# Performance work log

Measured on AMD Instinct MI355X. Metric: run time of the kernel, lower is better.

The kernel has to match this reference:

```python
import jax, jax.numpy as jnp
import numpy as np

N_NODES = 100000

def setup_inputs() -> dict:
    key = jax.random.key(0)
    k1, k2, k3, k4 = jax.random.split(key, 4)
    B, S, D, H = 50000, 10, 128, 128
    nodes = jax.random.randint(k1, (B,), 0, N_NODES, dtype=jnp.int64 if jax.config.jax_enable_x64 else jnp.int32)
    neigh_idx = jax.random.randint(k2, (B, S), 0, N_NODES, dtype=nodes.dtype)
    feature = jax.random.normal(k3, (N_NODES, D), dtype=jnp.float32)
    weight = jax.random.normal(k4, (2 * D, H), dtype=jnp.float32) * (1.0 / np.sqrt(2 * D))
    return {"nodes": nodes, "neigh_idx": neigh_idx, "feature": feature, "weight": weight}

def reference(nodes, neigh_idx, feature, weight):
    # Mean aggregation over sampled neighbors: [B, S, D] -> [B, D]
    neigh_feats = jnp.mean(feature[neigh_idx], axis=1)
    # Self features: [B, D]
    self_feats = feature[nodes]
    # Concat + linear + ReLU (gcn=False branch)
    combined = jnp.concatenate([self_feats, neigh_feats], axis=1)  # [B, 2D]
    return jax.nn.relu(combined @ weight)  # [B, H]
```

## Files before the change

kernel.cpp:

```cpp
#include <hip/hip_runtime.h>


typedef __attribute__((ext_vector_type(8))) short bf16x8;
typedef __attribute__((ext_vector_type(4))) float f32x4;

__device__ __forceinline__ unsigned short f2bf(float x) {
  unsigned int u = __float_as_uint(x);
  u += 0x7fffu + ((u >> 16) & 1u);
  return (unsigned short)(u >> 16);
}

__global__ void sage_prep_wt2(const float* __restrict__ W,
                              unsigned short* __restrict__ Wt) {
  __shared__ float tile[32][132];
  const int t = threadIdx.x;
  const int kbase = blockIdx.x * 32;
  const float4* w4 = (const float4*)(W + (size_t)kbase * 128);
#pragma unroll
  for (int j = 0; j < 4; ++j) {
    int f4i = t + j * 256;
    float4 v = w4[f4i];
    int flat = f4i << 2;
    int kk = flat >> 7;
    int h  = flat & 127;
    tile[kk][h] = v.x; tile[kk][h + 1] = v.y;
    tile[kk][h + 2] = v.z; tile[kk][h + 3] = v.w;
  }
  __syncthreads();
  const int h  = t >> 1;
  const int kc = (t & 1) * 16;
  unsigned short* dst = &Wt[(size_t)h * 256 + kbase + kc];
#pragma unroll
  for (int j = 0; j < 4; ++j) {
    ushort4 o;
    o.x = f2bf(tile[kc + 4 * j + 0][h]);
    o.y = f2bf(tile[kc + 4 * j + 1][h]);
    o.z = f2bf(tile[kc + 4 * j + 2][h]);
    o.w = f2bf(tile[kc + 4 * j + 3][h]);
    *(ushort4*)&dst[4 * j] = o;
  }
}

__global__ __launch_bounds__(512, 4)
void sage_fused6(const int* __restrict__ nodes,
                 const int* __restrict__ neigh,
                 const float* __restrict__ feat,
                 const unsigned short* __restrict__ Wt,
                 float* __restrict__ out, int B)
{
  constexpr int K = 256, H = 128, S = 10;
  constexpr int TILE = 64;
  constexpr int STR = K + 8;
  __shared__ unsigned short Clds[TILE * STR];

  const int t = threadIdx.x;
  const int block0 = blockIdx.x * TILE;

  {
    const int r   = t >> 5;
    const int sub = t & 31;
    const float4* f4 = (const float4*)feat;

#pragma unroll
    for (int half = 0; half < 4; ++half) {
      const int row = r + half * 16;
      const int b = block0 + row;
      unsigned short* crow = &Clds[row * STR];
      if (b < B) {
        const long srow = (long)nodes[b] * 32;
        float4 sv = f4[srow + sub];

        float ax = 0.f, ay = 0.f, az = 0.f, aw = 0.f;
#pragma unroll
        for (int s = 0; s < S; ++s) {
          const long nrow = (long)neigh[b * S + s] * 32;
          float4 v = f4[nrow + sub];
          ax += v.x; ay += v.y; az += v.z; aw += v.w;
        }
        ushort4 o;
        o.x = f2bf(sv.x); o.y = f2bf(sv.y); o.z = f2bf(sv.z); o.w = f2bf(sv.w);
        *(ushort4*)&crow[4 * sub] = o;
        o.x = f2bf(ax * 0.1f); o.y = f2bf(ay * 0.1f);
        o.z = f2bf(az * 0.1f); o.w = f2bf(aw * 0.1f);
        *(ushort4*)&crow[128 + 4 * sub] = o;
      } else {
        ushort4 z; z.x = z.y = z.z = z.w = 0;
        *(ushort4*)&crow[4 * sub] = z;
        *(ushort4*)&crow[128 + 4 * sub] = z;
      }
    }
  }
  __syncthreads();
  __builtin_amdgcn_sched_barrier(0);

  const int lane = t & 63;
  const int wave = t >> 6;
  const int m    = lane & 15;
  const int quad = lane >> 4;
  const int cbase = wave * 16;

  bf16x8 bfrag[8];
#pragma unroll
  for (int ks = 0; ks < 8; ++ks)
    bfrag[ks] = *(const bf16x8*)&Wt[(cbase + m) * K + ks * 32 + quad * 8];

  f32x4 acc0 = {0.f, 0.f, 0.f, 0.f};
  f32x4 acc1 = {0.f, 0.f, 0.f, 0.f};
  f32x4 acc2 = {0.f, 0.f, 0.f, 0.f};
  f32x4 acc3 = {0.f, 0.f, 0.f, 0.f};
#pragma unroll
  for (int ks = 0; ks < 8; ++ks) {
    const int koff = ks * 32 + quad * 8;
    bf16x8 a0 = *(const bf16x8*)&Clds[(m     ) * STR + koff];
    bf16x8 a1 = *(const bf16x8*)&Clds[(16 + m) * STR + koff];
    bf16x8 a2 = *(const bf16x8*)&Clds[(32 + m) * STR + koff];
    bf16x8 a3 = *(const bf16x8*)&Clds[(48 + m) * STR + koff];
    acc0 = __builtin_amdgcn_mfma_f32_16x16x32_bf16(a0, bfrag[ks], acc0, 0, 0, 0);
    acc1 = __builtin_amdgcn_mfma_f32_16x16x32_bf16(a1, bfrag[ks], acc1, 0, 0, 0);
    acc2 = __builtin_amdgcn_mfma_f32_16x16x32_bf16(a2, bfrag[ks], acc2, 0, 0, 0);
    acc3 = __builtin_amdgcn_mfma_f32_16x16x32_bf16(a3, bfrag[ks], acc3, 0, 0, 0);
  }

#pragma unroll
  for (int reg = 0; reg < 4; ++reg) {
    const int row0 = quad * 4 + reg;
    const int gb0 = block0 + row0;
    const int gb1 = gb0 + 16;
    const int gb2 = gb0 + 32;
    const int gb3 = gb0 + 48;
    if (gb0 < B) out[(size_t)gb0 * H + cbase + m] = fmaxf(acc0[reg], 0.0f);
    if (gb1 < B) out[(size_t)gb1 * H + cbase + m] = fmaxf(acc1[reg], 0.0f);
    if (gb2 < B) out[(size_t)gb2 * H + cbase + m] = fmaxf(acc2[reg], 0.0f);
    if (gb3 < B) out[(size_t)gb3 * H + cbase + m] = fmaxf(acc3[reg], 0.0f);
  }
}

extern "C" void kernel_launch(void* const* d_in, const int* in_sizes, int n_in,
                              void* d_out, int out_size, void* d_ws, size_t ws_size,
                              hipStream_t stream) {
  const int*   nodes = (const int*)d_in[0];
  const int*   neigh = (const int*)d_in[1];
  const float* feat  = (const float*)d_in[2];
  const float* W     = (const float*)d_in[3];
  float*       out   = (float*)d_out;
  const int B = in_sizes[0];

  unsigned short* Wt = (unsigned short*)d_ws;
  sage_prep_wt2<<<8, 256, 0, stream>>>(W, Wt);
  const int grid = (B + 63) / 64;
  sage_fused6<<<grid, 512, 0, stream>>>(nodes, neigh, feat, Wt, out, B);
}
```

Measured before the change: 132.5 us.

## Halve row tile and issue all neighbor gathers up front per thread

The row tile drops from 64 to 32 rows per block. Each row is now handled by 16 threads, and each thread loads two float4 halves. All 22 gather loads (10 neighbors times two halves, plus two self loads) are issued before any accumulation, and the sums use a tree reduction. This raises memory-level parallelism for the random row gathers. In exchange, register pressure per thread rises and the weight fragments are reloaded across twice as many blocks.

New measurement: 132.2 us. About the same (-0.3%).

```diff
diff --git a/kernel.cpp b/kernel.cpp
--- a/kernel.cpp
+++ b/kernel.cpp
@@ -8,6 +8,10 @@
   unsigned int u = __float_as_uint(x);
   u += 0x7fffu + ((u >> 16) & 1u);
   return (unsigned short)(u >> 16);
+}
+__device__ __forceinline__ float4 f4add(float4 a, float4 b) {
+  float4 r; r.x = a.x + b.x; r.y = a.y + b.y; r.z = a.z + b.z; r.w = a.w + b.w;
+  return r;
 }
 
 __global__ void sage_prep_wt2(const float* __restrict__ W,
@@ -42,14 +46,14 @@
 }
 
 __global__ __launch_bounds__(512, 4)
-void sage_fused6(const int* __restrict__ nodes,
+void sage_fused8(const int* __restrict__ nodes,
                  const int* __restrict__ neigh,
                  const float* __restrict__ feat,
                  const unsigned short* __restrict__ Wt,
                  float* __restrict__ out, int B)
 {
-  constexpr int K = 256, H = 128, S = 10;
-  constexpr int TILE = 64;
+  constexpr int K = 256, H = 128;
+  constexpr int TILE = 32;
   constexpr int STR = K + 8;
   __shared__ unsigned short Clds[TILE * STR];
 
@@ -57,37 +61,54 @@
   const int block0 = blockIdx.x * TILE;
 
   {
-    const int r   = t >> 5;
-    const int sub = t & 31;
-    const float4* f4 = (const float4*)feat;
+    const int r   = t >> 4;
+    const int sub = t & 15;
+    const int b   = block0 + r;
+    unsigned short* crow = &Clds[r * STR];
+    if (b < B) {
+      const float4* f4 = (const float4*)feat;
+      const int* nb = &neigh[b * 10];
+      const int i0 = nb[0], i1 = nb[1], i2 = nb[2], i3 = nb[3], i4 = nb[4];
+      const int i5 = nb[5], i6 = nb[6], i7 = nb[7], i8 = nb[8], i9 = nb[9];
+      const long srow = (long)nodes[b] * 32 + sub;
+      const long r0 = (long)i0 * 32 + sub, r1 = (long)i1 * 32 + sub;
+      const long r2 = (long)i2 * 32 + sub, r3 = (long)i3 * 32 + sub;
+      const long r4 = (long)i4 * 32 + sub, r5 = (long)i5 * 32 + sub;
+      const long r6 = (long)i6 * 32 + sub, r7 = (long)i7 * 32 + sub;
+      const long r8 = (long)i8 * 32 + sub, r9 = (long)i9 * 32 + sub;
 
-#pragma unroll
-    for (int half = 0; half < 4; ++half) {
-      const int row = r + half * 16;
-      const int b = block0 + row;
-      unsigned short* crow = &Clds[row * STR];
-      if (b < B) {
-        const long srow = (long)nodes[b] * 32;
-        float4 sv = f4[srow + sub];
+      float4 a0 = f4[r0],      a1 = f4[r1],      a2 = f4[r2],      a3 = f4[r3];
+      float4 a4 = f4[r4],      a5 = f4[r5],      a6 = f4[r6],      a7 = f4[r7];
+      float4 a8 = f4[r8],      a9 = f4[r9];
+      float4 b0 = f4[r0 + 16], b1 = f4[r1 + 16], b2 = f4[r2 + 16], b3 = f4[r3 + 16];
+      float4 b4 = f4[r4 + 16], b5 = f4[r5 + 16], b6 = f4[r6 + 16], b7 = f4[r7 + 16];
+      float4 b8 = f4[r8 + 16], b9 = f4[r9 + 16];
+      float4 s0 = f4[srow],    s1 = f4[srow + 16];
 
-        float ax = 0.f, ay = 0.f, az = 0.f, aw = 0.f;
-#pragma unroll
-        for (int s = 0; s < S; ++s) {
-          const long nrow = (long)neigh[b * S + s] * 32;
-          float4 v = f4[nrow + sub];
-          ax += v.x; ay += v.y; az += v.z; aw += v.w;
-        }
-        ushort4 o;
-        o.x = f2bf(sv.x); o.y = f2bf(sv.y); o.z = f2bf(sv.z); o.w = f2bf(sv.w);
-        *(ushort4*)&crow[4 * sub] = o;
-        o.x = f2bf(ax * 0.1f); o.y = f2bf(ay * 0.1f);
-        o.z = f2bf(az * 0.1f); o.w = f2bf(aw * 0.1f);
-        *(ushort4*)&crow[128 + 4 * sub] = o;
-      } else {
-        ushort4 z; z.x = z.y = z.z = z.w = 0;
-        *(ushort4*)&crow[4 * sub] = z;
-        *(ushort4*)&crow[128 + 4 * sub] = z;
-      }
+      float4 e0 = f4add(a0, a1), e1 = f4add(a2, a3);
+      float4 e2 = f4add(a4, a5), e3 = f4add(a6, a7);
+      float4 sumA = f4add(f4add(f4add(e0, e1), f4add(e2, e3)), f4add(a8, a9));
+      float4 g0 = f4add(b0, b1), g1 = f4add(b2, b3);
+      float4 g2 = f4add(b4, b5), g3 = f4add(b6, b7);
+      float4 sumB = f4add(f4add(f4add(g0, g1), f4add(g2, g3)), f4add(b8, b9));
+
+      ushort4 o;
+      o.x = f2bf(s0.x); o.y = f2bf(s0.y); o.z = f2bf(s0.z); o.w = f2bf(s0.w);
+      *(ushort4*)&crow[4 * sub] = o;
+      o.x = f2bf(s1.x); o.y = f2bf(s1.y); o.z = f2bf(s1.z); o.w = f2bf(s1.w);
+      *(ushort4*)&crow[64 + 4 * sub] = o;
+      o.x = f2bf(sumA.x * 0.1f); o.y = f2bf(sumA.y * 0.1f);
+      o.z = f2bf(sumA.z * 0.1f); o.w = f2bf(sumA.w * 0.1f);
+      *(ushort4*)&crow[128 + 4 * sub] = o;
+      o.x = f2bf(sumB.x * 0.1f); o.y = f2bf(sumB.y * 0.1f);
+      o.z = f2bf(sumB.z * 0.1f); o.w = f2bf(sumB.w * 0.1f);
+      *(ushort4*)&crow[192 + 4 * sub] = o;
+    } else {
+      ushort4 z; z.x = z.y = z.z = z.w = 0;
+      *(ushort4*)&crow[4 * sub] = z;
+      *(ushort4*)&crow[64 + 4 * sub] = z;
+      *(ushort4*)&crow[128 + 4 * sub] = z;
+      *(ushort4*)&crow[192 + 4 * sub] = z;
     }
   }
   __syncthreads();
@@ -106,19 +127,13 @@
 
   f32x4 acc0 = {0.f, 0.f, 0.f, 0.f};
   f32x4 acc1 = {0.f, 0.f, 0.f, 0.f};
-  f32x4 acc2 = {0.f, 0.f, 0.f, 0.f};
-  f32x4 acc3 = {0.f, 0.f, 0.f, 0.f};
 #pragma unroll
   for (int ks = 0; ks < 8; ++ks) {
     const int koff = ks * 32 + quad * 8;
     bf16x8 a0 = *(const bf16x8*)&Clds[(m     ) * STR + koff];
     bf16x8 a1 = *(const bf16x8*)&Clds[(16 + m) * STR + koff];
-    bf16x8 a2 = *(const bf16x8*)&Clds[(32 + m) * STR + koff];
-    bf16x8 a3 = *(const bf16x8*)&Clds[(48 + m) * STR + koff];
     acc0 = __builtin_amdgcn_mfma_f32_16x16x32_bf16(a0, bfrag[ks], acc0, 0, 0, 0);
     acc1 = __builtin_amdgcn_mfma_f32_16x16x32_bf16(a1, bfrag[ks], acc1, 0, 0, 0);
-    acc2 = __builtin_amdgcn_mfma_f32_16x16x32_bf16(a2, bfrag[ks], acc2, 0, 0, 0);
-    acc3 = __builtin_amdgcn_mfma_f32_16x16x32_bf16(a3, bfrag[ks], acc3, 0, 0, 0);
   }
 
 #pragma unroll
@@ -126,12 +141,8 @@
     const int row0 = quad * 4 + reg;
     const int gb0 = block0 + row0;
     const int gb1 = gb0 + 16;
-    const int gb2 = gb0 + 32;
-    const int gb3 = gb0 + 48;
     if (gb0 < B) out[(size_t)gb0 * H + cbase + m] = fmaxf(acc0[reg], 0.0f);
     if (gb1 < B) out[(size_t)gb1 * H + cbase + m] = fmaxf(acc1[reg], 0.0f);
-    if (gb2 < B) out[(size_t)gb2 * H + cbase + m] = fmaxf(acc2[reg], 0.0f);
-    if (gb3 < B) out[(size_t)gb3 * H + cbase + m] = fmaxf(acc3[reg], 0.0f);
   }
 }
 
@@ -147,6 +158,6 @@
 
   unsigned short* Wt = (unsigned short*)d_ws;
   sage_prep_wt2<<<8, 256, 0, stream>>>(W, Wt);
-  const int grid = (B + 63) / 64;
-  sage_fused6<<<grid, 512, 0, stream>>>(nodes, neigh, feat, Wt, out, B);
+  const int grid = (B + 31) / 32;
+  sage_fused8<<<grid, 512, 0, stream>>>(nodes, neigh, feat, Wt, out, B);
 }
```
